# Optimization experiments

Measured on AMD Instinct MI355X. Metric: run time of the kernel, lower is better.

## Reference

```python
import jax, jax.numpy as jnp
import numpy as np

B, L, C, H, W, R = 2, 16, 64, 64, 128, 32
MH = 32          # forcing MLP hidden
M1, M2 = 8, 8    # spectral conv modes


def _conv2d(x, w, b):
    # x: (N, C, H, W), w: (O, C, kh, kw), SAME padding
    y = jax.lax.conv_general_dilated(x, w, (1, 1), 'SAME',
                                     dimension_numbers=('NCHW', 'OIHW', 'NCHW'))
    return y + b[None, :, None, None]


def setup_inputs():
    k = jax.random.split(jax.random.key(0), 24)
    r_min, r_max = 0.8, 0.99
    u1 = jax.random.uniform(k[0], (C, R))
    u2 = jax.random.uniform(k[1], (C, R))
    nu_log = jnp.log(-0.5 * jnp.log(u1 * (r_max ** 2 - r_min ** 2) + r_min ** 2))
    theta_log = jnp.log(u2 * (2.0 * np.pi))
    s = np.float32(1.0 / np.sqrt(C))
    rn = lambda kk, sh, sc=1.0: np.float32(sc) * jax.random.normal(kk, sh, jnp.float32)
    return {
        'x': rn(k[2], (B, L, C, H, W)),
        'nu_log': nu_log.astype(jnp.float32),
        'theta_log': theta_log.astype(jnp.float32),
        'mlp_w1': rn(k[3], (C, MH), 0.02), 'mlp_b1': jnp.zeros((MH,), jnp.float32),
        'mlp_w2': rn(k[4], (MH, C * R * 2), 0.02), 'mlp_b2': jnp.zeros((C * R * 2,), jnp.float32),
        'forcing_scale': jnp.asarray(0.1, jnp.float32),
        'U_r': rn(k[5], (C, H, R), 1.0 / np.sqrt(H)), 'U_i': rn(k[6], (C, H, R), 1.0 / np.sqrt(H)),
        'V_r': rn(k[7], (C, W, R), 1.0 / np.sqrt(W)), 'V_i': rn(k[8], (C, W, R), 1.0 / np.sqrt(W)),
        'projW_r': rn(k[9], (C, C), s), 'projW_i': rn(k[10], (C, C), s),
        'projb_r': jnp.zeros((C,), jnp.float32), 'projb_i': jnp.zeros((C,), jnp.float32),
        'swr1': rn(k[11], (C, C, M1, M2), s), 'swi1': rn(k[12], (C, C, M1, M2), s),
        'swr2': rn(k[13], (C, C, M1, M2), s), 'swi2': rn(k[14], (C, C, M1, M2), s),
        'convr_w': rn(k[15], (C, C, 3, 3), 0.05), 'convr_b': jnp.zeros((C,), jnp.float32),
        'convi_w': rn(k[16], (C, C, 3, 3), 0.05), 'convi_b': jnp.zeros((C,), jnp.float32),
        'fuse_w': rn(k[17], (C, 2 * C), s), 'fuse_b': jnp.zeros((C,), jnp.float32),
        'gate_w': rn(k[18], (C, C), s), 'gate_b': jnp.zeros((C,), jnp.float32),
        'ln_w': jnp.ones((H, W), jnp.float32), 'ln_b': jnp.zeros((H, W), jnp.float32),
    }


def reference(x, nu_log, theta_log, mlp_w1, mlp_b1, mlp_w2, mlp_b2, forcing_scale,
              U_r, U_i, V_r, V_i, projW_r, projW_i, projb_r, projb_i,
              swr1, swi1, swr2, swi2, convr_w, convr_b, convi_w, convi_b,
              fuse_w, fuse_b, gate_w, gate_b, ln_w, ln_b):
    b_, l_, c_, h_, w_ = x.shape
    # --- selective forcing: spatial-mean context modulates LRU poles ---
    ctx = x.mean((-2, -1))                                       # (B,L,C)
    hmid = jnp.tanh(ctx @ mlp_w1 + mlp_b1)
    delta = (hmid @ mlp_w2 + mlp_b2).reshape(b_, l_, 2, c_, R)
    nu = jnp.exp(nu_log + forcing_scale * delta[:, :, 0])        # (B,L,C,R)
    th = jnp.exp(theta_log + forcing_scale * delta[:, :, 1])
    lam = jnp.exp(1j * th - nu)                                  # |lam| = exp(-nu) in (0,1)
    gamma = jnp.sqrt(1.0 - jnp.exp(-2.0 * nu))                   # input normalization
    # --- spectral encode + low-rank projection ---
    U = U_r + 1j * U_i                                           # (C,H,R)
    V = V_r + 1j * V_i                                           # (C,W,R)
    xf = jnp.fft.fft2(x)                                         # (B,L,C,H,W) complex64
    u = jnp.einsum('blchw,chr,cwr->blcr', xf, U, V)              # rank-R forcing
    # --- time-varying diagonal linear recurrence via parallel scan ---
    def comb(e1, e2):
        a1, b1 = e1
        a2, b2 = e2
        return a2 * a1, a2 * b1 + b2
    _, hstate = jax.lax.associative_scan(
        comb, (lam.astype(u.dtype), gamma.astype(u.dtype) * u), axis=1)
    # --- decode back to frequency grid, channel mix ---
    yf = jnp.einsum('blcr,chr,cwr->blchw', hstate, U, V)
    projW = projW_r + 1j * projW_i
    yf = jnp.einsum('blchw,oc->blohw', yf, projW) \
         + (projb_r + 1j * projb_i)[None, None, :, None, None]
    # --- spectral-conv frequency prior (low modes, both corners) ---
    w1 = swr1 + 1j * swi1
    w2 = swr2 + 1j * swi2
    sp = jnp.zeros_like(xf)
    sp = sp.at[:, :, :, :M1, :M2].set(
        jnp.einsum('blcxy,ocxy->bloxy', xf[:, :, :, :M1, :M2], w1))
    sp = sp.at[:, :, :, -M1:, :M2].set(
        jnp.einsum('blcxy,ocxy->bloxy', xf[:, :, :, -M1:, :M2], w2))
    yf = yf + sp
    # --- back to space, real/imag convs, fusion, LN, gate, residual ---
    y = jnp.fft.ifft2(yf)
    yr = _conv2d(y.real.reshape(b_ * l_, c_, h_, w_), convr_w, convr_b)
    yi = _conv2d(y.imag.reshape(b_ * l_, c_, h_, w_), convi_w, convi_b)
    fused = jnp.concatenate([yr, yi], axis=1).reshape(b_, l_, 2 * c_, h_, w_)
    out = jnp.einsum('blkhw,ok->blohw', fused, fuse_w) \
          + fuse_b[None, None, :, None, None]
    mu = out.mean((-2, -1), keepdims=True)
    var = out.var((-2, -1), keepdims=True)
    out = (out - mu) / jnp.sqrt(var + 1e-5) * ln_w + ln_b
    gate = jax.nn.sigmoid(jnp.einsum('blchw,oc->blohw', x, gate_w)
                          + gate_b[None, None, :, None, None])
    return x + gate * out
```

## Files before the change

### kernel.cpp

```cpp
#include <hip/hip_runtime.h>
#include <math.h>


constexpr int B_ = 2, L_ = 16, C = 64, H = 64, W = 128, R = 32, MH = 32;
constexpr int BL = B_ * L_;
constexpr int HW = H * W;
constexpr int CR = C * R;
constexpr float PI2 = 6.28318530717958647692f;

#define DEV __device__ __forceinline__

typedef __attribute__((ext_vector_type(8))) short bf16x8;
typedef __attribute__((ext_vector_type(4))) float f32x4;

static DEV unsigned short f2bf(float f) {
  unsigned u = __float_as_uint(f);
  u = u + 0x7fffu + ((u >> 16) & 1u);
  return (unsigned short)(u >> 16);
}

__global__ __launch_bounds__(128) void k_trig(float* __restrict__ t64,
                                              float* __restrict__ t128) {
  int i = threadIdx.x;
  if (i < 64) {
    float s, c; sincosf(PI2 * (float)i / 64.0f, &s, &c);
    t64[2 * i] = c; t64[2 * i + 1] = s;
  }
  float s, c; sincosf(PI2 * (float)i / 128.0f, &s, &c);
  t128[2 * i] = c; t128[2 * i + 1] = s;
}

__global__ __launch_bounds__(256) void k_utab(const float* __restrict__ Ur,
                                              const float* __restrict__ Ui,
                                              const float* __restrict__ t64,
                                              float* __restrict__ Uhat,
                                              float* __restrict__ Util) {
  int c = blockIdx.x;
  __shared__ float tt[128];
  if (threadIdx.x < 128) tt[threadIdx.x] = t64[threadIdx.x];
  __syncthreads();
  for (int t = 0; t < 8; t++) {
    int idx = t * 256 + threadIdx.x;
    int hp = idx >> 5, r = idx & 31;
    float fr = 0, fi = 0, br = 0, bi = 0;
    for (int h = 0; h < H; h++) {
      float ur = Ur[(c * H + h) * R + r], ui = Ui[(c * H + h) * R + r];
      int ph = (h * hp) & 63;
      float cs = tt[2 * ph], sn = tt[2 * ph + 1];
      fr += ur * cs + ui * sn;
      fi += ui * cs - ur * sn;
      br += ur * cs - ui * sn;
      bi += ui * cs + ur * sn;
    }
    int o = ((c * H + hp) * R + r) * 2;
    Uhat[o] = fr; Uhat[o + 1] = fi;
    Util[o] = br * (1.0f / H); Util[o + 1] = bi * (1.0f / H);
  }
}

__global__ __launch_bounds__(256) void k_vtab(const float* __restrict__ Vr,
                                              const float* __restrict__ Vi,
                                              const float* __restrict__ t128,
                                              float* __restrict__ Vhat,
                                              unsigned short* __restrict__ Vt2r,
                                              unsigned short* __restrict__ Vt2i) {
  int c = blockIdx.x;
  __shared__ float tt[256];
  tt[threadIdx.x] = t128[threadIdx.x];
  __syncthreads();
  for (int t = 0; t < 16; t++) {
    int idx = t * 256 + threadIdx.x;
    int wp = idx >> 5, r = idx & 31;
    float fr = 0, fi = 0, br = 0, bi = 0;
    for (int w = 0; w < W; w++) {
      float vr = Vr[(c * W + w) * R + r], vi = Vi[(c * W + w) * R + r];
      int ph = (w * wp) & 127;
      float cs = tt[2 * ph], sn = tt[2 * ph + 1];
      fr += vr * cs + vi * sn;
      fi += vi * cs - vr * sn;
      br += vr * cs - vi * sn;
      bi += vi * cs + vr * sn;
    }
    int of = ((c * W + wp) * R + r) * 2;
    Vhat[of] = fr; Vhat[of + 1] = fi;
    Vt2r[(size_t)(c * W + wp) * R + r] = f2bf(br * (1.0f / W));
    Vt2i[(size_t)(c * W + wp) * R + r] = f2bf(bi * (1.0f / W));
  }
}

__global__ __launch_bounds__(256) void k_wb(const float* __restrict__ fuse_w,
                                            const float* __restrict__ convr_w,
                                            const float* __restrict__ convi_w,
                                            unsigned short* __restrict__ Wb) {
  int po = blockIdx.x; int p = po >> 6, o = po & 63;
  const float* cw = p ? convi_w : convr_w;
  __shared__ float fw[64];
  if (threadIdx.x < 64) fw[threadIdx.x] = fuse_w[o * (2 * C) + p * C + threadIdx.x];
  __syncthreads();
  for (int t = 0; t < 3; t++) {
    int idx = t * 256 + threadIdx.x;
    if (idx < 576) {
      int tap = idx >> 6, c = idx & 63;
      float s = 0;
      for (int k = 0; k < C; k++) s += fw[k] * cw[(k * C + c) * 9 + tap];
      Wb[((size_t)(p * 9 + tap) * C + o) * C + c] = f2bf(s);
    }
  }
}

__global__ __launch_bounds__(64) void k_btil(const float* __restrict__ fuse_w,
                                             const float* __restrict__ rb,
                                             const float* __restrict__ ib,
                                             const float* __restrict__ fb,
                                             float* __restrict__ btil) {
  int o = threadIdx.x;
  float s = fb[o];
  for (int k = 0; k < C; k++)
    s += fuse_w[o * (2 * C) + k] * rb[k] + fuse_w[o * (2 * C) + C + k] * ib[k];
  btil[o] = s;
}

__global__ __launch_bounds__(128) void k_p2(const float* __restrict__ pwr,
                                            const float* __restrict__ pwi,
                                            unsigned short* __restrict__ P2) {
  int o = blockIdx.x;
  int k = threadIdx.x;
  int c = k >> 1, odd = k & 1;
  float pr = pwr[o * C + c], pi = pwi[o * C + c];
  float vr = odd ? -pi : pr;
  float vi = odd ? pr : pi;
  int boff = (k * 2) ^ ((o & 7) << 4);
  *(unsigned short*)((char*)P2 + o * 256 + boff) = f2bf(vr);
  *(unsigned short*)((char*)P2 + 16384 + o * 256 + boff) = f2bf(vi);
}

__global__ __launch_bounds__(256) void k_ctx(const float* __restrict__ x,
                                             float* __restrict__ ctx) {
  int blc = blockIdx.x;
  const float4* px = (const float4*)(x + (size_t)blc * HW);
  float s = 0;
  for (int i = threadIdx.x; i < HW / 4; i += 256) {
    float4 v = px[i];
    s += (v.x + v.y) + (v.z + v.w);
  }
  #pragma unroll
  for (int o2 = 32; o2; o2 >>= 1) s += __shfl_down(s, o2);
  __shared__ float red[4];
  if ((threadIdx.x & 63) == 0) red[threadIdx.x >> 6] = s;
  __syncthreads();
  if (threadIdx.x == 0)
    ctx[blc] = (red[0] + red[1] + red[2] + red[3]) * (1.0f / HW);
}

__global__ __launch_bounds__(256) void k_mlp(const float* __restrict__ ctx,
                                             const float* __restrict__ w1,
                                             const float* __restrict__ b1,
                                             const float* __restrict__ w2,
                                             const float* __restrict__ b2,
                                             const float* __restrict__ fs_p,
                                             const float* __restrict__ nu_log,
                                             const float* __restrict__ th_log,
                                             float* __restrict__ lamr,
                                             float* __restrict__ lami,
                                             float* __restrict__ gam) {
  int bl = blockIdx.x;
  __shared__ float cs[C];
  __shared__ float hm[MH];
  if (threadIdx.x < C) cs[threadIdx.x] = ctx[bl * C + threadIdx.x];
  __syncthreads();
  if (threadIdx.x < MH) {
    float s = b1[threadIdx.x];
    for (int k = 0; k < C; k++) s += cs[k] * w1[k * MH + threadIdx.x];
    hm[threadIdx.x] = tanhf(s);
  }
  __syncthreads();
  float fs = fs_p[0];
  for (int t = 0; t < 8; t++) {
    int idx = t * 256 + threadIdx.x;
    float d0 = b2[idx], d1 = b2[CR + idx];
    for (int m = 0; m < MH; m++) {
      float hv = hm[m];
      d0 += hv * w2[m * (2 * CR) + idx];
      d1 += hv * w2[m * (2 * CR) + CR + idx];
    }
    float nu = expf(nu_log[idx] + fs * d0);
    float th = expf(th_log[idx] + fs * d1);
    float en = expf(-nu);
    float sn, cn; sincosf(th, &sn, &cn);
    int o = bl * CR + idx;
    lamr[o] = en * cn; lami[o] = en * sn;
    gam[o] = sqrtf(fmaxf(0.0f, 1.0f - en * en));
  }
}

__global__ __launch_bounds__(256) void k_encode(const float* __restrict__ x,
                                                const float* __restrict__ Vhat,
                                                const float* __restrict__ Uhat,
                                                const float* __restrict__ t64,
                                                const float* __restrict__ t128,
                                                float* __restrict__ ub,
                                                float* __restrict__ Xm) {
  int blc = blockIdx.x;
  int c = blc & 63;
  __shared__ float sarr[H * R * 2];
  __shared__ float fh[16 * W * 2];
  int tid = threadIdx.x;
  const float* px = x + (size_t)blc * HW;
  {
    int rp = tid & 15, hb = tid >> 4;
    float ar[4][4];
    #pragma unroll
    for (int q = 0; q < 4; q++)
      for (int j = 0; j < 4; j++) ar[q][j] = 0;
    const float* vp = Vhat + ((size_t)c * W * R + 2 * rp) * 2;
    for (int ww = 0; ww < W; ww++) {
      float4 vv = *(const float4*)(vp + (size_t)ww * R * 2);
      #pragma unroll
      for (int q = 0; q < 4; q++) {
        float xv = px[(hb + 16 * q) * W + ww];
        ar[q][0] += xv * vv.x; ar[q][1] += xv * vv.y;
        ar[q][2] += xv * vv.z; ar[q][3] += xv * vv.w;
      }
    }
    #pragma unroll
    for (int q = 0; q < 4; q++) {
      int h = hb + 16 * q;
      *(float4*)&sarr[(h * R + 2 * rp) * 2] =
          make_float4(ar[q][0], ar[q][1], ar[q][2], ar[q][3]);
    }
  }
  __syncthreads();
  if (tid < R) {
    int r = tid;
    float ar = 0, ai = 0;
    const float* up = Uhat + ((size_t)c * H * R + r) * 2;
    for (int h2 = 0; h2 < H; h2++) {
      float sr = sarr[(h2 * R + r) * 2], si = sarr[(h2 * R + r) * 2 + 1];
      float ur = up[(size_t)h2 * R * 2], ui2 = up[(size_t)h2 * R * 2 + 1];
      ar += ur * sr - ui2 * si;
      ai += ur * si + ui2 * sr;
    }
    ub[((size_t)blc * R + r) * 2] = ar;
    ub[((size_t)blc * R + r) * 2 + 1] = ai;
  }
  {
    int wq = tid & 127, ip = tid >> 7;
    for (int t = 0; t < 8; t++) {
      int i1 = t * 2 + ip;
      int m1 = i1 < 8 ? i1 : 48 + i1;
      float fr = 0, fi = 0;
      for (int h2 = 0; h2 < H; h2++) {
        float xv = px[h2 * W + wq];
        int ph = (m1 * h2) & 63;
        fr += xv * t64[2 * ph];
        fi -= xv * t64[2 * ph + 1];
      }
      fh[(i1 * W + wq) * 2] = fr; fh[(i1 * W + wq) * 2 + 1] = fi;
    }
  }
  __syncthreads();
  if (tid < 128) {
    int i1 = tid >> 3, m2 = tid & 7;
    float ar = 0, ai = 0;
    for (int ww = 0; ww < W; ww++) {
      float fr = fh[(i1 * W + ww) * 2], fi = fh[(i1 * W + ww) * 2 + 1];
      int ph = (m2 * ww) & 127;
      float cs = t128[2 * ph], sn = t128[2 * ph + 1];
      ar += fr * cs + fi * sn;
      ai += fi * cs - fr * sn;
    }
    Xm[((size_t)blc * 128 + tid) * 2] = ar;
    Xm[((size_t)blc * 128 + tid) * 2 + 1] = ai;
  }
}

__global__ __launch_bounds__(256) void k_scan(const float* __restrict__ lamr,
                                              const float* __restrict__ lami,
                                              const float* __restrict__ gam,
                                              const float* __restrict__ ub,
                                              float* __restrict__ hs) {
  int idx = blockIdx.x * 256 + threadIdx.x;
  int b = idx >> 11, cr = idx & 2047;
  float hr = 0, hi = 0;
  for (int l = 0; l < L_; l++) {
    int o = (b * L_ + l) * CR + cr;
    float lr = lamr[o], li = lami[o], g = gam[o];
    float ur = ub[2 * o], ui = ub[2 * o + 1];
    float nr = lr * hr - li * hi + g * ur;
    float ni = lr * hi + li * hr + g * ui;
    hr = nr; hi = ni;
    hs[2 * o] = hr; hs[2 * o + 1] = hi;
  }
}

__global__ __launch_bounds__(256) void k_spm(const float* __restrict__ Xm,
                                             const float* __restrict__ w1r,
                                             const float* __restrict__ w1i,
                                             const float* __restrict__ w2r,
                                             const float* __restrict__ w2i,
                                             float* __restrict__ SPm) {
  int bl = blockIdx.x;
  int o0 = blockIdx.y * 8;
  const float* px = Xm + (size_t)bl * C * 256;
  for (int t = 0; t < 4; t++) {
    int idx = t * 256 + threadIdx.x;
    int o = o0 + (idx >> 7), mode = idx & 127;
    int i1 = mode >> 3, m2 = mode & 7;
    const float* wr; const float* wi; int ii;
    if (i1 < 8) { wr = w1r; wi = w1i; ii = i1; }
    else        { wr = w2r; wi = w2i; ii = i1 - 8; }
    float ar = 0, ai = 0;
    for (int cc = 0; cc < C; cc++) {
      float xr = px[(cc * 128 + mode) * 2], xi = px[(cc * 128 + mode) * 2 + 1];
      float wrr = wr[((size_t)(o * C + cc) * 8 + ii) * 8 + m2];
      float wii = wi[((size_t)(o * C + cc) * 8 + ii) * 8 + m2];
      ar += xr * wrr - xi * wii;
      ai += xr * wii + xi * wrr;
    }
    size_t oo = (size_t)bl * C * 128 + (size_t)o * 128 + mode;
    SPm[oo * 2] = ar * (1.0f / HW);
    SPm[oo * 2 + 1] = ai * (1.0f / HW);
  }
}

__global__ __launch_bounds__(256) void k_q(const float* __restrict__ SPm,
                                           const float* __restrict__ t64,
                                           float* __restrict__ Qb) {
  int blo = blockIdx.x;
  __shared__ float sp[256];
  int tid = threadIdx.x;
  sp[tid] = SPm[(size_t)blo * 256 + tid];
  __syncthreads();
  for (int t = 0; t < 2; t++) {
    int idx = t * 256 + tid;
    int h = idx >> 3, m2 = idx & 7;
    float ar = 0, ai = 0;
    #pragma unroll
    for (int i1 = 0; i1 < 16; i1++) {
      int m1 = i1 < 8 ? i1 : 48 + i1;
      int ph = (m1 * h) & 63;
      float cs = t64[2 * ph], sn = t64[2 * ph + 1];
      float sr = sp[(i1 * 8 + m2) * 2], si = sp[(i1 * 8 + m2) * 2 + 1];
      ar += sr * cs - si * sn;
      ai += sr * sn + si * cs;
    }
    Qb[((size_t)blo * H * 8 + idx) * 2] = ar;
    Qb[((size_t)blo * H * 8 + idx) * 2 + 1] = ai;
  }
}

__global__ __launch_bounds__(256) void k_y(
    const float* __restrict__ hs, const float* __restrict__ Util,
    const unsigned short* __restrict__ Vt2r,
    const unsigned short* __restrict__ Vt2i,
    unsigned* __restrict__ y2) {
  int bl = blockIdx.x;
  int h0 = blockIdx.y * 16;
  int zz = blockIdx.z;
  int w0 = (zz >> 4) * 64;
  int chunk = zz & 15;
  int tid = threadIdx.x;
  int lane = tid & 63;
  int wv = __builtin_amdgcn_readfirstlane(tid >> 6);
  __shared__ unsigned ybuf[1024 * 4];
  int row = lane & 15;
  int kg = lane >> 4;
  int c = chunk * 4 + wv;
  const float* up = Util + (((size_t)c * H + h0 + row) * R + kg * 8) * 2;
  const float* hp = hs + (((size_t)bl * C + c) * R + kg * 8) * 2;
  bf16x8 aGr, aGi, aGn;
  #pragma unroll
  for (int j = 0; j < 8; j++) {
    float ur = up[2 * j], ui = up[2 * j + 1];
    float hr = hp[2 * j], hi = hp[2 * j + 1];
    float gr = hr * ur - hi * ui, gi = hr * ui + hi * ur;
    aGr[j] = (short)f2bf(gr); aGi[j] = (short)f2bf(gi);
    aGn[j] = (short)f2bf(-gi);
  }
  #pragma unroll
  for (int nt = 0; nt < 4; nt++) {
    int w = w0 + nt * 16 + row;
    const unsigned short* vr = Vt2r + ((size_t)c * W + w) * R + kg * 8;
    const unsigned short* vi = Vt2i + ((size_t)c * W + w) * R + kg * 8;
    bf16x8 bVr = *(const bf16x8*)vr;
    bf16x8 bVi = *(const bf16x8*)vi;
    f32x4 accr = {0, 0, 0, 0}, acci = {0, 0, 0, 0};
    accr = __builtin_amdgcn_mfma_f32_16x16x32_bf16(aGr, bVr, accr, 0, 0, 0);
    accr = __builtin_amdgcn_mfma_f32_16x16x32_bf16(aGn, bVi, accr, 0, 0, 0);
    acci = __builtin_amdgcn_mfma_f32_16x16x32_bf16(aGr, bVi, acci, 0, 0, 0);
    acci = __builtin_amdgcn_mfma_f32_16x16x32_bf16(aGi, bVr, acci, 0, 0, 0);
    #pragma unroll
    for (int r = 0; r < 4; r++) {
      int hl = kg * 4 + r;
      unsigned pk = (unsigned)f2bf(accr[r]) | ((unsigned)f2bf(acci[r]) << 16);
      ybuf[(hl * 64 + nt * 16 + row) * 4 + wv] = pk;
    }
  }
  __syncthreads();
  #pragma unroll
  for (int q = 0; q < 4; q++) {
    int p = q * 256 + tid;
    int lh = p >> 6, lw = p & 63;
    uint4 v = *(const uint4*)&ybuf[p * 4];
    size_t pixg = ((size_t)bl * H + h0 + lh) * W + (w0 + lw);
    int off = (chunk * 16) ^ ((lw & 7) << 4);
    *(uint4*)((char*)y2 + pixg * 256 + off) = v;
  }
}

__global__ __launch_bounds__(256) void k_proj(
    const unsigned* __restrict__ y2, const unsigned short* __restrict__ P2,
    const float* __restrict__ Qb, const float* __restrict__ pbr,
    const float* __restrict__ pbi, const float* __restrict__ t128,
    unsigned short* __restrict__ Zr, unsigned short* __restrict__ Zi) {
  int bl = blockIdx.x;
  int h = blockIdx.y;
  int tid = threadIdx.x, lane = tid & 63;
  int wv = __builtin_amdgcn_readfirstlane(tid >> 6);
  __shared__ __align__(16) char ylds[32768];
  __shared__ __align__(16) char plds[32768];
  {
    const uint4* gy = (const uint4*)((const char*)y2 +
                                     ((size_t)bl * H + h) * W * 256);
    const uint4* gp = (const uint4*)P2;
    uint4* ly = (uint4*)ylds; uint4* lp = (uint4*)plds;
    for (int i = tid; i < 2048; i += 256) ly[i] = gy[i];
    for (int i = tid; i < 2048; i += 256) lp[i] = gp[i];
  }
  __syncthreads();
  int col = lane & 15, kg = lane >> 4;
  f32x4 zr[4][2], zi[4][2];
  #pragma unroll
  for (int mt = 0; mt < 4; mt++)
    for (int nt = 0; nt < 2; nt++) { zr[mt][nt] = (f32x4){0,0,0,0}; zi[mt][nt] = (f32x4){0,0,0,0}; }
  #pragma unroll
  for (int ks = 0; ks < 4; ks++) {
    int koff = ks * 64 + kg * 16;
    bf16x8 ar[4], ai[4];
    #pragma unroll
    for (int mt = 0; mt < 4; mt++) {
      int o = mt * 16 + col;
      int ab = o * 256 + (koff ^ ((o & 7) << 4));
      ar[mt] = *(const bf16x8*)(plds + ab);
      ai[mt] = *(const bf16x8*)(plds + 16384 + ab);
    }
    #pragma unroll
    for (int nt = 0; nt < 2; nt++) {
      int pix = wv * 32 + nt * 16 + col;
      bf16x8 b = *(const bf16x8*)(ylds + pix * 256 + (koff ^ ((pix & 7) << 4)));
      #pragma unroll
      for (int mt = 0; mt < 4; mt++) {
        zr[mt][nt] = __builtin_amdgcn_mfma_f32_16x16x32_bf16(ar[mt], b, zr[mt][nt], 0, 0, 0);
        zi[mt][nt] = __builtin_amdgcn_mfma_f32_16x16x32_bf16(ai[mt], b, zi[mt][nt], 0, 0, 0);
      }
    }
  }
  #pragma unroll
  for (int nt = 0; nt < 2; nt++) {
    int w = wv * 32 + nt * 16 + col;
    float csv[8], snv[8];
    #pragma unroll
    for (int m2 = 0; m2 < 8; m2++) {
      int ph = (m2 * w) & 127;
      csv[m2] = t128[2 * ph]; snv[m2] = t128[2 * ph + 1];
    }
    #pragma unroll
    for (int mt = 0; mt < 4; mt++) {
      float vrr[4], vii[4];
      #pragma unroll
      for (int r = 0; r < 4; r++) {
        int o = mt * 16 + kg * 4 + r;
        const float* qp = Qb + ((size_t)(bl * C + o) * H + h) * 16;
        float vr = zr[mt][nt][r], vi = zi[mt][nt][r];
        #pragma unroll
        for (int m2 = 0; m2 < 8; m2++) {
          float qr = qp[2 * m2], qi = qp[2 * m2 + 1];
          vr += qr * csv[m2] - qi * snv[m2];
          vi += qr * snv[m2] + qi * csv[m2];
        }
        if (h == 0 && w == 0) { vr += pbr[o]; vi += pbi[o]; }
        vrr[r] = vr; vii[r] = vi;
      }
      size_t zoff = (((size_t)bl * H + h) * W + w) * C + mt * 16 + kg * 4;
      unsigned p0 = f2bf(vrr[0]) | ((unsigned)f2bf(vrr[1]) << 16);
      unsigned p1 = f2bf(vrr[2]) | ((unsigned)f2bf(vrr[3]) << 16);
      *(uint2*)(Zr + zoff) = make_uint2(p0, p1);
      unsigned q0 = f2bf(vii[0]) | ((unsigned)f2bf(vii[1]) << 16);
      unsigned q1 = f2bf(vii[2]) | ((unsigned)f2bf(vii[3]) << 16);
      *(uint2*)(Zi + zoff) = make_uint2(q0, q1);
    }
  }
}

__global__ __launch_bounds__(256) void k_conv(const unsigned short* __restrict__ Zr,
                                              const unsigned short* __restrict__ Zi,
                                              const unsigned short* __restrict__ Wb,
                                              const float* __restrict__ btil,
                                              float* __restrict__ outp) {
  int bl = blockIdx.x >> 6;
  int h = blockIdx.x & 63;
  int tid = threadIdx.x;
  int lane = tid & 63;
  int wv = __builtin_amdgcn_readfirstlane(tid >> 6);
  __shared__ __align__(16) char zs[130 * 128];
  f32x4 acc[4][2];
  #pragma unroll
  for (int mt = 0; mt < 4; mt++)
    for (int nt = 0; nt < 2; nt++) acc[mt][nt] = (f32x4){0, 0, 0, 0};

  for (int p = 0; p < 2; p++) {
    const unsigned short* Z = p ? Zi : Zr;
    for (int dh = 0; dh < 3; dh++) {
      int hr = h + dh - 1;
      __syncthreads();
      if (hr >= 0 && hr < H) {
        const uint4* src = (const uint4*)(Z + ((size_t)(bl * H + hr)) * W * C);
        #pragma unroll
        for (int i = 0; i < 4; i++) {
          int ch = tid * 4 + i;
          int ws = 1 + (ch >> 3), c2 = (ch & 7) * 16;
          int byte = (ws * 128 + c2) ^ ((ws & 7) << 4);
          *(uint4*)(zs + byte) = src[ch];
        }
      } else {
        #pragma unroll
        for (int i = 0; i < 4; i++) {
          int ch = tid * 4 + i;
          int ws = 1 + (ch >> 3), c2 = (ch & 7) * 16;
          int byte = (ws * 128 + c2) ^ ((ws & 7) << 4);
          *(uint4*)(zs + byte) = make_uint4(0, 0, 0, 0);
        }
      }
      if (tid < 16) {
        int ws = (tid < 8) ? 0 : 129; int c2 = (tid & 7) * 16;
        int byte = (ws * 128 + c2) ^ ((ws & 7) << 4);
        *(uint4*)(zs + byte) = make_uint4(0, 0, 0, 0);
      }
      __syncthreads();
      #pragma unroll
      for (int kc = 0; kc < 2; kc++) {
        #pragma unroll
        for (int dw = 0; dw < 3; dw++) {
          int tap = dh * 3 + dw;
          bf16x8 bfr[2];
          #pragma unroll
          for (int nt = 0; nt < 2; nt++) {
            int ws = wv * 32 + nt * 16 + (lane & 15) + dw;
            int byte = (ws * 128 + (kc * 32 + (lane >> 4) * 8) * 2) ^ ((ws & 7) << 4);
            bfr[nt] = *(const bf16x8*)(zs + byte);
          }
          const unsigned short* wbp =
              Wb + ((size_t)(p * 9 + tap) * C) * C + kc * 32 + (lane >> 4) * 8;
          #pragma unroll
          for (int mt = 0; mt < 4; mt++) {
            bf16x8 af = *(const bf16x8*)(wbp + (size_t)(mt * 16 + (lane & 15)) * C);
            acc[mt][0] = __builtin_amdgcn_mfma_f32_16x16x32_bf16(af, bfr[0], acc[mt][0], 0, 0, 0);
            acc[mt][1] = __builtin_amdgcn_mfma_f32_16x16x32_bf16(af, bfr[1], acc[mt][1], 0, 0, 0);
          }
        }
      }
    }
  }
  #pragma unroll
  for (int mt = 0; mt < 4; mt++) {
    #pragma unroll
    for (int nt = 0; nt < 2; nt++) {
      int w = wv * 32 + nt * 16 + (lane & 15);
      #pragma unroll
      for (int r = 0; r < 4; r++) {
        int o = mt * 16 + (lane >> 4) * 4 + r;
        outp[((size_t)(bl * C + o) * H + h) * W + w] = acc[mt][nt][r] + btil[o];
      }
    }
  }
}

__global__ __launch_bounds__(256) void k_lnstats(const float* __restrict__ outp,
                                                 float* __restrict__ mu,
                                                 float* __restrict__ rstd) {
  int i = blockIdx.x;
  const float4* p = (const float4*)(outp + (size_t)i * HW);
  float s = 0, q = 0;
  for (int t = threadIdx.x; t < HW / 4; t += 256) {
    float4 v = p[t];
    s += (v.x + v.y) + (v.z + v.w);
    q += (v.x * v.x + v.y * v.y) + (v.z * v.z + v.w * v.w);
  }
  #pragma unroll
  for (int o2 = 32; o2; o2 >>= 1) { s += __shfl_down(s, o2); q += __shfl_down(q, o2); }
  __shared__ float rs[4], rq[4];
  if ((threadIdx.x & 63) == 0) { rs[threadIdx.x >> 6] = s; rq[threadIdx.x >> 6] = q; }
  __syncthreads();
  if (threadIdx.x == 0) {
    float S = rs[0] + rs[1] + rs[2] + rs[3];
    float Q = rq[0] + rq[1] + rq[2] + rq[3];
    float m = S * (1.0f / HW);
    float var = Q * (1.0f / HW) - m * m;
    mu[i] = m; rstd[i] = rsqrtf(var + 1e-5f);
  }
}

__global__ __launch_bounds__(256) void k_final(const float* __restrict__ x,
                                               const float* __restrict__ gw,
                                               const float* __restrict__ gb,
                                               const float* __restrict__ mu,
                                               const float* __restrict__ rstd,
                                               const float* __restrict__ lnw,
                                               const float* __restrict__ lnb,
                                               float* __restrict__ outp) {
  int bl = blockIdx.x >> 6, h = blockIdx.x & 63;
  int tid = threadIdx.x;
  __shared__ float xs[C * W];
  for (int i = tid; i < C * W; i += 256) {
    int c = i >> 7, w = i & 127;
    xs[i] = x[((size_t)(bl * C + c) * H + h) * W + w];
  }
  __syncthreads();
  int w = tid & 127;
  int oh = __builtin_amdgcn_readfirstlane(tid >> 7);
  float glin[32];
  #pragma unroll
  for (int i = 0; i < 32; i++) glin[i] = gb[oh * 32 + i];
  for (int cc = 0; cc < C; cc++) {
    float xv = xs[cc * W + w];
    const float* gwp = gw + (size_t)(oh * 32) * C + cc;
    #pragma unroll
    for (int i = 0; i < 32; i++) glin[i] += gwp[(size_t)i * C] * xv;
  }
  float lw = lnw[h * W + w], lb = lnb[h * W + w];
  #pragma unroll
  for (int i = 0; i < 32; i++) {
    int o = oh * 32 + i;
    size_t off = ((size_t)(bl * C + o) * H + h) * W + w;
    float m = mu[bl * C + o], rs = rstd[bl * C + o];
    float op = outp[off];
    float nrm = (op - m) * rs * lw + lb;
    float sg = 1.0f / (1.0f + expf(-glin[i]));
    outp[off] = xs[o * W + w] + sg * nrm;
  }
}

extern "C" void kernel_launch(void* const* d_in, const int* in_sizes, int n_in,
                              void* d_out, int out_size, void* d_ws,
                              size_t ws_size, hipStream_t stream) {
  const float* x       = (const float*)d_in[0];
  const float* nu_log  = (const float*)d_in[1];
  const float* th_log  = (const float*)d_in[2];
  const float* mlp_w1  = (const float*)d_in[3];
  const float* mlp_b1  = (const float*)d_in[4];
  const float* mlp_w2  = (const float*)d_in[5];
  const float* mlp_b2  = (const float*)d_in[6];
  const float* fscale  = (const float*)d_in[7];
  const float* U_r     = (const float*)d_in[8];
  const float* U_i     = (const float*)d_in[9];
  const float* V_r     = (const float*)d_in[10];
  const float* V_i     = (const float*)d_in[11];
  const float* pW_r    = (const float*)d_in[12];
  const float* pW_i    = (const float*)d_in[13];
  const float* pb_r    = (const float*)d_in[14];
  const float* pb_i    = (const float*)d_in[15];
  const float* swr1    = (const float*)d_in[16];
  const float* swi1    = (const float*)d_in[17];
  const float* swr2    = (const float*)d_in[18];
  const float* swi2    = (const float*)d_in[19];
  const float* convr_w = (const float*)d_in[20];
  const float* convr_b = (const float*)d_in[21];
  const float* convi_w = (const float*)d_in[22];
  const float* convi_b = (const float*)d_in[23];
  const float* fuse_w  = (const float*)d_in[24];
  const float* fuse_b  = (const float*)d_in[25];
  const float* gate_w  = (const float*)d_in[26];
  const float* gate_b  = (const float*)d_in[27];
  const float* ln_w    = (const float*)d_in[28];
  const float* ln_b    = (const float*)d_in[29];
  float* outp = (float*)d_out;

  char* wsb = (char*)d_ws;
  size_t off = 0;
  auto alloc = [&](size_t nbytes) -> void* {
    void* p = (void*)(wsb + off);
    off += ((nbytes + 255) / 256) * 256;
    return p;
  };
  float* trig64  = (float*)alloc(128 * 4);
  float* trig128 = (float*)alloc(256 * 4);
  float* Uhat = (float*)alloc((size_t)C * H * R * 2 * 4);
  float* Util = (float*)alloc((size_t)C * H * R * 2 * 4);
  float* Vhat = (float*)alloc((size_t)C * W * R * 2 * 4);
  unsigned short* Vt2r = (unsigned short*)alloc((size_t)C * W * R * 2);
  unsigned short* Vt2i = (unsigned short*)alloc((size_t)C * W * R * 2);
  unsigned short* Wb = (unsigned short*)alloc((size_t)2 * 9 * C * C * 2);
  float* btil = (float*)alloc(C * 4);
  unsigned short* P2 = (unsigned short*)alloc((size_t)2 * C * 128 * 2);
  float* ctx  = (float*)alloc(BL * C * 4);
  float* lamr = (float*)alloc(BL * CR * 4);
  float* lami = (float*)alloc(BL * CR * 4);
  float* gam  = (float*)alloc(BL * CR * 4);
  float* ub   = (float*)alloc((size_t)BL * CR * 2 * 4);
  float* hs   = (float*)alloc((size_t)BL * CR * 2 * 4);
  float* Xm   = (float*)alloc((size_t)BL * C * 128 * 2 * 4);
  float* SPm  = (float*)alloc((size_t)BL * C * 128 * 2 * 4);
  float* Qb   = (float*)alloc((size_t)BL * C * H * 8 * 2 * 4);
  unsigned* y2 = (unsigned*)alloc((size_t)BL * HW * C * 4);
  unsigned short* Zr = (unsigned short*)alloc((size_t)BL * HW * C * 2);
  unsigned short* Zi = (unsigned short*)alloc((size_t)BL * HW * C * 2);
  float* mu   = (float*)alloc(BL * C * 4);
  float* rstd = (float*)alloc(BL * C * 4);

  k_trig<<<1, 128, 0, stream>>>(trig64, trig128);
  k_utab<<<C, 256, 0, stream>>>(U_r, U_i, trig64, Uhat, Util);
  k_vtab<<<C, 256, 0, stream>>>(V_r, V_i, trig128, Vhat, Vt2r, Vt2i);
  k_wb<<<2 * C, 256, 0, stream>>>(fuse_w, convr_w, convi_w, Wb);
  k_btil<<<1, 64, 0, stream>>>(fuse_w, convr_b, convi_b, fuse_b, btil);
  k_p2<<<C, 128, 0, stream>>>(pW_r, pW_i, P2);
  k_ctx<<<BL * C, 256, 0, stream>>>(x, ctx);
  k_mlp<<<BL, 256, 0, stream>>>(ctx, mlp_w1, mlp_b1, mlp_w2, mlp_b2, fscale,
                                nu_log, th_log, lamr, lami, gam);
  k_encode<<<BL * C, 256, 0, stream>>>(x, Vhat, Uhat, trig64, trig128, ub, Xm);
  k_scan<<<16, 256, 0, stream>>>(lamr, lami, gam, ub, hs);
  k_spm<<<dim3(BL, 8), 256, 0, stream>>>(Xm, swr1, swi1, swr2, swi2, SPm);
  k_q<<<BL * C, 256, 0, stream>>>(SPm, trig64, Qb);
  k_y<<<dim3(BL, 4, 32), 256, 0, stream>>>(hs, Util, Vt2r, Vt2i, y2);
  k_proj<<<dim3(BL, H), 256, 0, stream>>>(y2, P2, Qb, pb_r, pb_i, trig128,
                                          Zr, Zi);
  k_conv<<<BL * H, 256, 0, stream>>>(Zr, Zi, Wb, btil, outp);
  k_lnstats<<<BL * C, 256, 0, stream>>>(outp, mu, rstd);
  k_final<<<BL * H, 256, 0, stream>>>(x, gate_w, gate_b, mu, rstd, ln_w, ln_b,
                                      outp);
}
```

Before: 1.057 ms.

## Rewrite encode with bf16 MFMA projections and fuse channel-mean into it

The encode kernel now stages each x plane in LDS as bf16 (row-major and transposed) and computes the V projection and the H-direction low-mode DFT with MFMA 16x16x32 bf16 instructions, replacing scalar fp32 loops. Vhat is stored as a bf16 K-major table and a new DFT-basis table Ehat is built in k_trig. The separate ctx reduction kernel is removed and the mean is computed during the same x load, saving one full read of x. The remaining U projection and W-direction DFT are re-parallelised across all threads with shuffle reductions. Using bf16 inputs lowers precision of the encoded coefficients.

```diff
diff --git a/kernel.cpp b/kernel.cpp
--- a/kernel.cpp
+++ b/kernel.cpp
@@ -20,7 +20,8 @@
 }
 
 __global__ __launch_bounds__(128) void k_trig(float* __restrict__ t64,
-                                              float* __restrict__ t128) {
+                                              float* __restrict__ t128,
+                                              unsigned short* __restrict__ Ehat) {
   int i = threadIdx.x;
   if (i < 64) {
     float s, c; sincosf(PI2 * (float)i / 64.0f, &s, &c);
@@ -28,6 +29,15 @@
   }
   float s, c; sincosf(PI2 * (float)i / 128.0f, &s, &c);
   t128[2 * i] = c; t128[2 * i + 1] = s;
+  for (int j = 0; j < 16; j++) {
+    int idx = j * 128 + i;
+    int row = idx >> 6, hh = idx & 63;
+    int i1 = row & 15, p = row >> 4;
+    int m1 = i1 < 8 ? i1 : 48 + i1;
+    float ang = PI2 * (float)((m1 * hh) & 63) / 64.0f;
+    float s2, c2; sincosf(ang, &s2, &c2);
+    Ehat[row * 64 + hh] = f2bf(p ? -s2 : c2);
+  }
 }
 
 __global__ __launch_bounds__(256) void k_utab(const float* __restrict__ Ur,
@@ -61,7 +71,7 @@
 __global__ __launch_bounds__(256) void k_vtab(const float* __restrict__ Vr,
                                               const float* __restrict__ Vi,
                                               const float* __restrict__ t128,
-                                              float* __restrict__ Vhat,
+                                              unsigned short* __restrict__ Vhb,
                                               unsigned short* __restrict__ Vt2r,
                                               unsigned short* __restrict__ Vt2i) {
   int c = blockIdx.x;
@@ -81,8 +91,8 @@
       br += vr * cs - vi * sn;
       bi += vi * cs + vr * sn;
     }
-    int of = ((c * W + wp) * R + r) * 2;
-    Vhat[of] = fr; Vhat[of + 1] = fi;
+    Vhb[((size_t)c * 64 + 2 * r) * 128 + wp] = f2bf(fr);
+    Vhb[((size_t)c * 64 + 2 * r + 1) * 128 + wp] = f2bf(fi);
     Vt2r[(size_t)(c * W + wp) * R + r] = f2bf(br * (1.0f / W));
     Vt2i[(size_t)(c * W + wp) * R + r] = f2bf(bi * (1.0f / W));
   }
@@ -132,24 +142,6 @@
   int boff = (k * 2) ^ ((o & 7) << 4);
   *(unsigned short*)((char*)P2 + o * 256 + boff) = f2bf(vr);
   *(unsigned short*)((char*)P2 + 16384 + o * 256 + boff) = f2bf(vi);
-}
-
-__global__ __launch_bounds__(256) void k_ctx(const float* __restrict__ x,
-                                             float* __restrict__ ctx) {
-  int blc = blockIdx.x;
-  const float4* px = (const float4*)(x + (size_t)blc * HW);
-  float s = 0;
-  for (int i = threadIdx.x; i < HW / 4; i += 256) {
-    float4 v = px[i];
-    s += (v.x + v.y) + (v.z + v.w);
-  }
-  #pragma unroll
-  for (int o2 = 32; o2; o2 >>= 1) s += __shfl_down(s, o2);
-  __shared__ float red[4];
-  if ((threadIdx.x & 63) == 0) red[threadIdx.x >> 6] = s;
-  __syncthreads();
-  if (threadIdx.x == 0)
-    ctx[blc] = (red[0] + red[1] + red[2] + red[3]) * (1.0f / HW);
 }
 
 __global__ __launch_bounds__(256) void k_mlp(const float* __restrict__ ctx,
@@ -193,84 +185,140 @@
   }
 }
 
-__global__ __launch_bounds__(256) void k_encode(const float* __restrict__ x,
-                                                const float* __restrict__ Vhat,
-                                                const float* __restrict__ Uhat,
-                                                const float* __restrict__ t64,
-                                                const float* __restrict__ t128,
-                                                float* __restrict__ ub,
-                                                float* __restrict__ Xm) {
+__global__ __launch_bounds__(256) void k_encode(
+    const float* __restrict__ x, const unsigned short* __restrict__ Vhb,
+    const float* __restrict__ Uhat, const unsigned short* __restrict__ Ehat,
+    const float* __restrict__ t128, float* __restrict__ ub,
+    float* __restrict__ Xm, float* __restrict__ ctx) {
   int blc = blockIdx.x;
   int c = blc & 63;
-  __shared__ float sarr[H * R * 2];
-  __shared__ float fh[16 * W * 2];
+  __shared__ __align__(16) char ldsA[16384];
+  __shared__ __align__(16) char ldsB[16384];
+  __shared__ float red[4];
   int tid = threadIdx.x;
-  const float* px = x + (size_t)blc * HW;
+  int lane = tid & 63;
+  int wv = __builtin_amdgcn_readfirstlane(tid >> 6);
+  int col = lane & 15, kg = lane >> 4;
+
+  const float4* px4 = (const float4*)(x + (size_t)blc * HW);
+  float csum = 0;
+  #pragma unroll
+  for (int j = 0; j < 8; j++) {
+    int e4 = j * 256 + tid;
+    float4 v = px4[e4];
+    csum += (v.x + v.y) + (v.z + v.w);
+    int elem = e4 * 4;
+    int h = elem >> 7, w = elem & 127;
+    unsigned p0 = (unsigned)f2bf(v.x) | ((unsigned)f2bf(v.y) << 16);
+    unsigned p1 = (unsigned)f2bf(v.z) | ((unsigned)f2bf(v.w) << 16);
+    int ba = (h * 256 + w * 2) ^ ((h & 7) << 4);
+    *(uint2*)(ldsA + ba) = make_uint2(p0, p1);
+    unsigned short t0 = f2bf(v.x), t1 = f2bf(v.y), t2 = f2bf(v.z), t3 = f2bf(v.w);
+    *(unsigned short*)(ldsB + (((w + 0) * 128 + h * 2) ^ (((w + 0) & 7) << 4))) = t0;
+    *(unsigned short*)(ldsB + (((w + 1) * 128 + h * 2) ^ (((w + 1) & 7) << 4))) = t1;
+    *(unsigned short*)(ldsB + (((w + 2) * 128 + h * 2) ^ (((w + 2) & 7) << 4))) = t2;
+    *(unsigned short*)(ldsB + (((w + 3) * 128 + h * 2) ^ (((w + 3) & 7) << 4))) = t3;
+  }
+  #pragma unroll
+  for (int m = 32; m; m >>= 1) csum += __shfl_xor(csum, m);
+  if (lane == 0) red[wv] = csum;
+  __syncthreads();
+  if (tid == 0)
+    ctx[blc] = (red[0] + red[1] + red[2] + red[3]) * (1.0f / HW);
+
+  f32x4 acc1[4];
+  #pragma unroll
+  for (int nt = 0; nt < 4; nt++) acc1[nt] = (f32x4){0, 0, 0, 0};
+  int hA = wv * 16 + col;
+  #pragma unroll
+  for (int ks = 0; ks < 4; ks++) {
+    int k0 = ks * 32 + kg * 8;
+    bf16x8 a = *(const bf16x8*)(ldsA + ((hA * 256 + k0 * 2) ^ ((hA & 7) << 4)));
+    #pragma unroll
+    for (int nt = 0; nt < 4; nt++) {
+      int n = nt * 16 + col;
+      bf16x8 b = *(const bf16x8*)(Vhb + ((size_t)c * 64 + n) * 128 + k0);
+      acc1[nt] = __builtin_amdgcn_mfma_f32_16x16x32_bf16(a, b, acc1[nt], 0, 0, 0);
+    }
+  }
+  f32x4 acc2[2][2];
+  #pragma unroll
+  for (int mt = 0; mt < 2; mt++)
+    for (int nt = 0; nt < 2; nt++) acc2[mt][nt] = (f32x4){0, 0, 0, 0};
+  #pragma unroll
+  for (int ks = 0; ks < 2; ks++) {
+    int k0 = ks * 32 + kg * 8;
+    bf16x8 a2[2];
+    #pragma unroll
+    for (int mt = 0; mt < 2; mt++)
+      a2[mt] = *(const bf16x8*)(Ehat + (mt * 16 + col) * 64 + k0);
+    #pragma unroll
+    for (int nt = 0; nt < 2; nt++) {
+      int w = wv * 32 + nt * 16 + col;
+      bf16x8 b2 = *(const bf16x8*)(ldsB + ((w * 128 + k0 * 2) ^ ((w & 7) << 4)));
+      #pragma unroll
+      for (int mt = 0; mt < 2; mt++)
+        acc2[mt][nt] = __builtin_amdgcn_mfma_f32_16x16x32_bf16(a2[mt], b2, acc2[mt][nt], 0, 0, 0);
+    }
+  }
+  __syncthreads();
+  #pragma unroll
+  for (int nt = 0; nt < 4; nt++) {
+    int r2 = nt * 16 + col;
+    #pragma unroll
+    for (int j = 0; j < 4; j++) {
+      int h = wv * 16 + kg * 4 + j;
+      *(float*)(ldsA + ((h * 256 + r2 * 4) ^ ((h & 7) << 4))) = acc1[nt][j];
+    }
+  }
+  #pragma unroll
+  for (int mt = 0; mt < 2; mt++)
+    for (int nt = 0; nt < 2; nt++)
+      #pragma unroll
+      for (int j = 0; j < 4; j++) {
+        int mrow = mt * 16 + kg * 4 + j;
+        int w = wv * 32 + nt * 16 + col;
+        *(float*)(ldsB + ((mrow * 512 + w * 4) ^ ((mrow & 7) << 4))) = acc2[mt][nt][j];
+      }
+  __syncthreads();
+
   {
-    int rp = tid & 15, hb = tid >> 4;
-    float ar[4][4];
-    #pragma unroll
-    for (int q = 0; q < 4; q++)
-      for (int j = 0; j < 4; j++) ar[q][j] = 0;
-    const float* vp = Vhat + ((size_t)c * W * R + 2 * rp) * 2;
-    for (int ww = 0; ww < W; ww++) {
-      float4 vv = *(const float4*)(vp + (size_t)ww * R * 2);
-      #pragma unroll
-      for (int q = 0; q < 4; q++) {
-        float xv = px[(hb + 16 * q) * W + ww];
-        ar[q][0] += xv * vv.x; ar[q][1] += xv * vv.y;
-        ar[q][2] += xv * vv.z; ar[q][3] += xv * vv.w;
-      }
-    }
-    #pragma unroll
-    for (int q = 0; q < 4; q++) {
-      int h = hb + 16 * q;
-      *(float4*)&sarr[(h * R + 2 * rp) * 2] =
-          make_float4(ar[q][0], ar[q][1], ar[q][2], ar[q][3]);
-    }
-  }
-  __syncthreads();
-  if (tid < R) {
-    int r = tid;
+    int r = tid >> 3, hg = tid & 7;
     float ar = 0, ai = 0;
-    const float* up = Uhat + ((size_t)c * H * R + r) * 2;
-    for (int h2 = 0; h2 < H; h2++) {
-      float sr = sarr[(h2 * R + r) * 2], si = sarr[(h2 * R + r) * 2 + 1];
-      float ur = up[(size_t)h2 * R * 2], ui2 = up[(size_t)h2 * R * 2 + 1];
-      ar += ur * sr - ui2 * si;
-      ai += ur * si + ui2 * sr;
-    }
-    ub[((size_t)blc * R + r) * 2] = ar;
-    ub[((size_t)blc * R + r) * 2 + 1] = ai;
+    #pragma unroll
+    for (int j = 0; j < 8; j++) {
+      int h = hg + 8 * j;
+      float2 sv = *(const float2*)(ldsA + ((h * 256 + r * 8) ^ ((h & 7) << 4)));
+      const float* up = Uhat + (((size_t)c * H + h) * R + r) * 2;
+      float ur = up[0], ui = up[1];
+      ar += ur * sv.x - ui * sv.y;
+      ai += ur * sv.y + ui * sv.x;
+    }
+    ar += __shfl_xor(ar, 1); ai += __shfl_xor(ai, 1);
+    ar += __shfl_xor(ar, 2); ai += __shfl_xor(ai, 2);
+    ar += __shfl_xor(ar, 4); ai += __shfl_xor(ai, 4);
+    if (hg == 0) {
+      ub[((size_t)blc * R + r) * 2] = ar;
+      ub[((size_t)blc * R + r) * 2 + 1] = ai;
+    }
   }
   {
-    int wq = tid & 127, ip = tid >> 7;
-    for (int t = 0; t < 8; t++) {
-      int i1 = t * 2 + ip;
-      int m1 = i1 < 8 ? i1 : 48 + i1;
-      float fr = 0, fi = 0;
-      for (int h2 = 0; h2 < H; h2++) {
-        float xv = px[h2 * W + wq];
-        int ph = (m1 * h2) & 63;
-        fr += xv * t64[2 * ph];
-        fi -= xv * t64[2 * ph + 1];
-      }
-      fh[(i1 * W + wq) * 2] = fr; fh[(i1 * W + wq) * 2 + 1] = fi;
-    }
-  }
-  __syncthreads();
-  if (tid < 128) {
-    int i1 = tid >> 3, m2 = tid & 7;
+    int i1 = tid >> 4, m2 = (tid >> 1) & 7, half = tid & 1;
     float ar = 0, ai = 0;
-    for (int ww = 0; ww < W; ww++) {
-      float fr = fh[(i1 * W + ww) * 2], fi = fh[(i1 * W + ww) * 2 + 1];
-      int ph = (m2 * ww) & 127;
+    for (int jw = 0; jw < 64; jw++) {
+      int w = half * 64 + jw;
+      float fr = *(const float*)(ldsB + ((i1 * 512 + w * 4) ^ ((i1 & 7) << 4)));
+      float fi = *(const float*)(ldsB + (((16 + i1) * 512 + w * 4) ^ ((i1 & 7) << 4)));
+      int ph = (m2 * w) & 127;
       float cs = t128[2 * ph], sn = t128[2 * ph + 1];
       ar += fr * cs + fi * sn;
       ai += fi * cs - fr * sn;
     }
-    Xm[((size_t)blc * 128 + tid) * 2] = ar;
-    Xm[((size_t)blc * 128 + tid) * 2 + 1] = ai;
+    ar += __shfl_xor(ar, 1); ai += __shfl_xor(ai, 1);
+    if (half == 0) {
+      Xm[((size_t)blc * 128 + i1 * 8 + m2) * 2] = ar;
+      Xm[((size_t)blc * 128 + i1 * 8 + m2) * 2 + 1] = ai;
+    }
   }
 }
 
@@ -684,9 +732,10 @@
   };
   float* trig64  = (float*)alloc(128 * 4);
   float* trig128 = (float*)alloc(256 * 4);
+  unsigned short* Ehat = (unsigned short*)alloc(32 * 64 * 2);
   float* Uhat = (float*)alloc((size_t)C * H * R * 2 * 4);
   float* Util = (float*)alloc((size_t)C * H * R * 2 * 4);
-  float* Vhat = (float*)alloc((size_t)C * W * R * 2 * 4);
+  unsigned short* Vhb = (unsigned short*)alloc((size_t)C * 64 * 128 * 2);
   unsigned short* Vt2r = (unsigned short*)alloc((size_t)C * W * R * 2);
   unsigned short* Vt2i = (unsigned short*)alloc((size_t)C * W * R * 2);
   unsigned short* Wb = (unsigned short*)alloc((size_t)2 * 9 * C * C * 2);
@@ -707,16 +756,15 @@
   float* mu   = (float*)alloc(BL * C * 4);
   float* rstd = (float*)alloc(BL * C * 4);
 
-  k_trig<<<1, 128, 0, stream>>>(trig64, trig128);
+  k_trig<<<1, 128, 0, stream>>>(trig64, trig128, Ehat);
   k_utab<<<C, 256, 0, stream>>>(U_r, U_i, trig64, Uhat, Util);
-  k_vtab<<<C, 256, 0, stream>>>(V_r, V_i, trig128, Vhat, Vt2r, Vt2i);
+  k_vtab<<<C, 256, 0, stream>>>(V_r, V_i, trig128, Vhb, Vt2r, Vt2i);
   k_wb<<<2 * C, 256, 0, stream>>>(fuse_w, convr_w, convi_w, Wb);
   k_btil<<<1, 64, 0, stream>>>(fuse_w, convr_b, convi_b, fuse_b, btil);
   k_p2<<<C, 128, 0, stream>>>(pW_r, pW_i, P2);
-  k_ctx<<<BL * C, 256, 0, stream>>>(x, ctx);
+  k_encode<<<BL * C, 256, 0, stream>>>(x, Vhb, Uhat, Ehat, trig128, ub, Xm, ctx);
   k_mlp<<<BL, 256, 0, stream>>>(ctx, mlp_w1, mlp_b1, mlp_w2, mlp_b2, fscale,
                                 nu_log, th_log, lamr, lami, gam);
-  k_encode<<<BL * C, 256, 0, stream>>>(x, Vhat, Uhat, trig64, trig128, ub, Xm);
   k_scan<<<16, 256, 0, stream>>>(lamr, lami, gam, ub, hs);
   k_spm<<<dim3(BL, 8), 256, 0, stream>>>(Xm, swr1, swi1, swr2, swi2, SPm);
   k_q<<<BL * C, 256, 0, stream>>>(SPm, trig64, Qb);
```

After: 881.2 us. 16.6% less time.
